# Kernel optimization log

Measured on AMD Instinct MI355X. Metric: run time of the kernel, lower is better.

The kernel has to match this reference:

```python
import jax, jax.numpy as jnp
import numpy as np

B, N, D, E = 8, 96, 512, 4
ALPHA = 0.2  # LeakyReLU negative slope (init arg `alpha`)


def setup_inputs() -> dict:
    key = jax.random.key(0)
    ks = jax.random.split(key, 12)
    nodes = jax.random.normal(ks[0], (B, N, D), jnp.float32)
    # edges[0]: in-edge type weights, edges[1]: out-edge type weights, each [E, D, D]
    edges = jax.random.normal(ks[1], (2, E, D, D), jnp.float32) * 0.05
    adj_in_type = jax.random.randint(ks[2], (B, N, N), 0, E)
    adj_out_type = jax.random.randint(ks[3], (B, N, N), 0, E)
    eye = jnp.eye(N, dtype=bool)  # self-loop guarantees no all-masked softmax row
    exist_in = (jax.random.uniform(ks[4], (B, N, N)) < 0.1) | eye
    exist_out = (jax.random.uniform(ks[5], (B, N, N)) < 0.1) | eye
    Wa_in = jax.random.normal(ks[6], (2 * D, 1), jnp.float32) * 0.02
    ba_in = jnp.zeros((1,), jnp.float32)
    Wa_out = jax.random.normal(ks[7], (2 * D, 1), jnp.float32) * 0.02
    ba_out = jnp.zeros((1,), jnp.float32)
    Wr = jax.random.normal(ks[8], (3 * D, D), jnp.float32) * 0.02
    br = jnp.zeros((D,), jnp.float32)
    Wz = jax.random.normal(ks[9], (3 * D, D), jnp.float32) * 0.02
    bz = jnp.zeros((D,), jnp.float32)
    Wh = jax.random.normal(ks[10], (3 * D, D), jnp.float32) * 0.02
    bh = jnp.zeros((D,), jnp.float32)
    return dict(nodes=nodes, edges=edges, adj_in_type=adj_in_type, adj_out_type=adj_out_type,
                exist_in=exist_in, exist_out=exist_out, Wa_in=Wa_in, ba_in=ba_in,
                Wa_out=Wa_out, ba_out=ba_out, Wr=Wr, br=br, Wz=Wz, bz=bz, Wh=Wh, bh=bh)


def _edge_messages(nodes, W_types, adj_type, exist):
    """msgs[b,i,j] = nodes[b,j] @ W_types[adj_type[b,i,j]] if edge (i<-j) exists else 0.
    Vectorizes the original triple Python loop: transform all nodes by all E edge
    types once, then gather per (b,i,j). nodes [B,N,D], W_types [E,D,D]."""
    all_msgs = jnp.einsum('bjh,ehd->bejd', nodes, W_types)  # [B,E,N,D]
    b_idx = jnp.arange(nodes.shape[0])[:, None, None]
    j_idx = jnp.arange(nodes.shape[1])[None, None, :]
    msgs = all_msgs[b_idx, adj_type, j_idx]                 # [B,N,N,D]
    return jnp.where(exist[..., None], msgs, 0.0)


def _graph_attention(node_h, msgs, exist, Wa, ba):
    """GAT over the N neighbor slots of each node (softmax along last N axis).
    node_h [B,N,D] is broadcast to pairs, matching node_hidden.unsqueeze(2).repeat."""
    h_rep = jnp.broadcast_to(node_h[:, :, None, :], msgs.shape)  # [B,N,N,D]
    feat = jnp.concatenate([h_rep, msgs], axis=-1)               # [B,N,N,2D]
    score = jax.nn.leaky_relu((feat @ Wa)[..., 0] + ba[0], ALPHA)  # [B,N,N]
    score = jnp.where(exist, score, -1e9)
    attn = jax.nn.softmax(score, axis=-1)
    return jnp.einsum('bij,bijd->bid', attn, msgs)               # [B,N,D]


def reference(nodes, edges, adj_in_type, adj_out_type, exist_in, exist_out,
              Wa_in, ba_in, Wa_out, ba_out, Wr, br, Wz, bz, Wh, bh):
    msgs_in = _edge_messages(nodes, edges[0], adj_in_type, exist_in)
    msgs_out = _edge_messages(nodes, edges[1], adj_out_type, exist_out)
    in_h = _graph_attention(nodes, msgs_in, exist_in, Wa_in, ba_in)
    out_h = _graph_attention(nodes, msgs_out, exist_out, Wa_out, ba_out)
    # Propagator: GGNN-style gated fusion of nodes with in/out aggregates
    a = jnp.concatenate([in_h, out_h], axis=-1)      # [B,N,2D]
    az = jnp.concatenate([a, nodes], axis=-1)        # [B,N,3D]
    r = jax.nn.sigmoid(az @ Wr + br)
    z = jax.nn.sigmoid(az @ Wz + bz)
    h_hat = jnp.tanh(jnp.concatenate([a, r * nodes], axis=-1) @ Wh + bh)
    return (1.0 - z) * nodes + z * h_hat
```

## Files before the change

kernel.cpp:

```cpp
#include <hip/hip_runtime.h>
#include <hip/hip_bf16.h>

#define BB 8
#define NN 96
#define DD 512
#define EE 4
#define ROWS 768

typedef __attribute__((ext_vector_type(8))) short s8v;
typedef __attribute__((ext_vector_type(4))) short s4v;
typedef __attribute__((ext_vector_type(4))) float f32x4;

#define WS_PROJP   4096
#define WS_NODESH  1048576
#define WS_ALLMSGS 2097152
#define WS_ACAT    8388608
#define WS_EDGEST  10747904
#define WS_WT      14942208
#define WS_RN      19660800
#define WS_ZB      20447232
#define WS_HPRE    22020096

__device__ __forceinline__ short f2bf(float x) {
  unsigned int u = __builtin_bit_cast(unsigned int, x);
  u += 0x7FFFu + ((u >> 16) & 1u);
  return (short)(u >> 16);
}
__device__ __forceinline__ float b2f(short s) {
  unsigned int u = ((unsigned int)(unsigned short)s) << 16;
  return __builtin_bit_cast(float, u);
}

__device__ __forceinline__ f32x4 mfma16(s8v a, s8v b, f32x4 c) {
  asm("v_mfma_f32_16x16x32_bf16 %0, %1, %2, %0" : "+v"(c) : "v"(a), "v"(b));
  return c;
}

__device__ __forceinline__ int get_exist(const void* p, int code, int idx) {
  switch (code) {
    case 0: return ((const unsigned char*)p)[idx] != 0;
    case 1: return ((const int*)p)[idx] != 0;
    case 2: return ((const float*)p)[idx] != 0.0f;
    default: return ((const long long*)p)[idx] != 0;
  }
}

__global__ __launch_bounds__(256) void k_prep(const float* __restrict__ edges,
                                              const float* __restrict__ Wr,
                                              const float* __restrict__ Wz,
                                              const float* __restrict__ Wh,
                                              const float* __restrict__ nodes,
                                              const void* exist_in,
                                              const void* exist_out,
                                              short* __restrict__ edgesT,
                                              short* __restrict__ WT,
                                              short* __restrict__ nodesH,
                                              short* __restrict__ AcatH,
                                              int* __restrict__ flags) {
  __shared__ float t[32][33];
  __shared__ int red[3];
  int z = blockIdx.z;
  if (z == 0) {
    if (blockIdx.x) return;
    int tt = threadIdx.x;
    int y = blockIdx.y;
    if (y < 2) {
      if (tt < 3) red[tt] = 0;
      __syncthreads();
      const uint4* p = (const uint4*)(y ? exist_out : exist_in);
      int mis = 0, gt = 0, od = 0;
      for (int i = tt; i < 4608; i += 256) {
        uint4 v = p[i];
        unsigned any = v.x | v.y | v.z | v.w;
        if (any) {
          if (any & 0xFFFFFF00u) mis = 1;
          if (any & 0xFEFEFEFEu) gt = 1;
          if (v.y | v.w) od = 1;
        }
      }
      if (mis) atomicOr(&red[0], 1);
      if (gt) atomicOr(&red[1], 1);
      if (od) atomicOr(&red[2], 1);
      __syncthreads();
      if (tt == 0) flags[y] = red[0] ? (red[1] ? 2 : 0) : (red[2] ? 1 : 3);
    } else if (y < 14) {
      int r0 = (y - 2) * 64;
      int c4 = (tt & 127) * 4;
#pragma unroll 4
      for (int p2 = 0; p2 < 32; ++p2) {
        int row = r0 + p2 * 2 + (tt >> 7);
        float4 v = *(const float4*)(nodes + (size_t)row * DD + c4);
        s4v o;
        o[0] = f2bf(v.x); o[1] = f2bf(v.y); o[2] = f2bf(v.z); o[3] = f2bf(v.w);
        *(s4v*)(nodesH + (size_t)row * DD + c4) = o;
        *(s4v*)(AcatH + (size_t)row * 1536 + 1024 + c4) = o;
      }
    }
    return;
  }
  const float* src;
  short* dst;
  int dstPitch;
  if (z < 9) {
    if (blockIdx.y >= 16) return;
    int e = z - 1;
    src = edges + (size_t)e * DD * DD;
    dst = edgesT + (size_t)e * DD * DD;
    dstPitch = DD;
  } else {
    int w = z - 9;
    src = w == 0 ? Wr : (w == 1 ? Wz : Wh);
    dst = WT + (size_t)w * (512 * 1536);
    dstPitch = 1536;
  }
  int r0 = blockIdx.y * 32, c0 = blockIdx.x * 32;
  int row = threadIdx.x >> 3, c4 = (threadIdx.x & 7) * 4;
  float4 v = *(const float4*)(src + (size_t)(r0 + row) * DD + c0 + c4);
  t[row][c4] = v.x; t[row][c4 + 1] = v.y; t[row][c4 + 2] = v.z; t[row][c4 + 3] = v.w;
  __syncthreads();
  s4v o;
  o[0] = f2bf(t[c4 + 0][row]); o[1] = f2bf(t[c4 + 1][row]);
  o[2] = f2bf(t[c4 + 2][row]); o[3] = f2bf(t[c4 + 3][row]);
  *(s4v*)(dst + (size_t)(c0 + row) * dstPitch + r0 + c4) = o;
}

__device__ __forceinline__ void mfma_tile(const short* As, const short* Bs,
                                          int wr, int wc, int l, f32x4 acc[2][2]) {
  int lr = l & 15, lg = l >> 4;
#pragma unroll
  for (int ks = 0; ks < 64; ks += 32) {
    s8v a0 = *(const s8v*)&As[(wr + lr) * 72 + ks + 8 * lg];
    s8v a1 = *(const s8v*)&As[(wr + 16 + lr) * 72 + ks + 8 * lg];
    s8v b0 = *(const s8v*)&Bs[(wc + lr) * 72 + ks + 8 * lg];
    s8v b1 = *(const s8v*)&Bs[(wc + 16 + lr) * 72 + ks + 8 * lg];
    acc[0][0] = mfma16(a0, b0, acc[0][0]);
    acc[0][1] = mfma16(a0, b1, acc[0][1]);
    acc[1][0] = mfma16(a1, b0, acc[1][0]);
    acc[1][1] = mfma16(a1, b1, acc[1][1]);
  }
}

__global__ __launch_bounds__(256) void k_gemm_msgs(const short* __restrict__ nodesH,
                                                   const short* __restrict__ edgesT,
                                                   const float* __restrict__ Wa_in,
                                                   const float* __restrict__ Wa_out,
                                                   short* __restrict__ C,
                                                   float* __restrict__ projp) {
  __shared__ __align__(16) short As[128 * 72];
  __shared__ __align__(16) short Bs[128 * 72];
  __shared__ float pp[2][128];
  int tid = threadIdx.x;
  int row0 = blockIdx.y * 128;
  int col0 = blockIdx.x * 128;
  int de = col0 >> 9, h0 = col0 & 511;
  int w = tid >> 6, l = tid & 63;
  int wr = (w >> 1) * 64, wc = (w & 1) * 64;
  int lr = l & 15, lg = l >> 4;
  int srow = tid >> 1, sc = (tid & 1) * 32;
  const short* Ap = nodesH + (size_t)(row0 + srow) * DD + sc;
  const short* Bp = edgesT + (size_t)de * DD * DD + (size_t)(h0 + srow) * DD + sc;
  s8v a0 = *(const s8v*)Ap, a1 = *(const s8v*)(Ap + 8);
  s8v a2 = *(const s8v*)(Ap + 16), a3 = *(const s8v*)(Ap + 24);
  s8v b0 = *(const s8v*)Bp, b1 = *(const s8v*)(Bp + 8);
  s8v b2 = *(const s8v*)(Bp + 16), b3 = *(const s8v*)(Bp + 24);
  f32x4 acc[4][4] = {};
  for (int k0 = 0; k0 < DD; k0 += 64) {
    *(s8v*)&As[srow * 72 + sc] = a0;      *(s8v*)&As[srow * 72 + sc + 8] = a1;
    *(s8v*)&As[srow * 72 + sc + 16] = a2; *(s8v*)&As[srow * 72 + sc + 24] = a3;
    *(s8v*)&Bs[srow * 72 + sc] = b0;      *(s8v*)&Bs[srow * 72 + sc + 8] = b1;
    *(s8v*)&Bs[srow * 72 + sc + 16] = b2; *(s8v*)&Bs[srow * 72 + sc + 24] = b3;
    __syncthreads();
    if (k0 + 64 < DD) {
      Ap += 64; Bp += 64;
      a0 = *(const s8v*)Ap; a1 = *(const s8v*)(Ap + 8);
      a2 = *(const s8v*)(Ap + 16); a3 = *(const s8v*)(Ap + 24);
      b0 = *(const s8v*)Bp; b1 = *(const s8v*)(Bp + 8);
      b2 = *(const s8v*)(Bp + 16); b3 = *(const s8v*)(Bp + 24);
    }
#pragma unroll
    for (int ks = 0; ks < 64; ks += 32) {
      s8v af[4], bf[4];
#pragma unroll
      for (int f = 0; f < 4; ++f) {
        af[f] = *(const s8v*)&As[(wr + f * 16 + lr) * 72 + ks + 8 * lg];
        bf[f] = *(const s8v*)&Bs[(wc + f * 16 + lr) * 72 + ks + 8 * lg];
      }
#pragma unroll
      for (int fi = 0; fi < 4; ++fi)
#pragma unroll
        for (int fj = 0; fj < 4; ++fj)
          acc[fi][fj] = mfma16(af[fi], bf[fj], acc[fi][fj]);
    }
    __syncthreads();
  }
  asm volatile("s_nop 7\n\ts_nop 7");
  int lg4 = lg * 4;
#pragma unroll
  for (int fi = 0; fi < 4; ++fi)
#pragma unroll
    for (int fj = 0; fj < 4; ++fj) {
      f32x4 v = acc[fi][fj];
#pragma unroll
      for (int r = 0; r < 4; ++r) {
        int row = row0 + wr + fi * 16 + lg4 + r;
        int col = h0 + wc + fj * 16 + lr;
        C[((size_t)(de * ROWS + row)) * DD + col] = f2bf(v[r]);
      }
    }
  const float* wa2 = ((de >> 2) ? Wa_out : Wa_in) + DD;
  float wv[4];
#pragma unroll
  for (int fj = 0; fj < 4; ++fj) wv[fj] = wa2[h0 + wc + fj * 16 + lr];
  float pr[4][4];
#pragma unroll
  for (int fi = 0; fi < 4; ++fi)
#pragma unroll
    for (int r = 0; r < 4; ++r) {
      float s = 0.f;
#pragma unroll
      for (int fj = 0; fj < 4; ++fj) s = fmaf(acc[fi][fj][r], wv[fj], s);
      pr[fi][r] = s;
    }
#pragma unroll
  for (int off = 1; off < 16; off <<= 1)
#pragma unroll
    for (int fi = 0; fi < 4; ++fi)
#pragma unroll
      for (int r = 0; r < 4; ++r) pr[fi][r] += __shfl_xor(pr[fi][r], off);
  if (lr == 0) {
#pragma unroll
    for (int fi = 0; fi < 4; ++fi)
#pragma unroll
      for (int r = 0; r < 4; ++r)
        pp[w & 1][(wr >> 6) * 64 + ((wr & 63) + fi * 16 + lg4 + r)] = pr[fi][r];
  }
  __syncthreads();
  if (tid < 128)
    projp[(size_t)(blockIdx.x & 3) * 6144 + de * ROWS + row0 + tid] =
        pp[0][tid] + pp[1][tid];
}

__global__ __launch_bounds__(256) void k_attn(const short* __restrict__ allmsgsH,
                                              const float* __restrict__ projp,
                                              const int* __restrict__ adj_in,
                                              const int* __restrict__ adj_out,
                                              const void* exist_in,
                                              const void* exist_out,
                                              const int* __restrict__ fr,
                                              const float* __restrict__ nodes,
                                              const float* __restrict__ Wa_in,
                                              const float* __restrict__ ba_in,
                                              const float* __restrict__ Wa_out,
                                              const float* __restrict__ ba_out,
                                              short* __restrict__ AcatH) {
  __shared__ float s_w[NN];
  __shared__ int s_off[NN];
  __shared__ int s_list[NN];
  __shared__ int s_cnt[2];
  __shared__ float s_part[5];
  int blk = blockIdx.x;
  int dir = blk / ROWS;
  int row = blk % ROWS;
  int b = row / NN;
  const int* adj = dir ? adj_out : adj_in;
  const void* ex = dir ? exist_out : exist_in;
  int code = fr[dir];
  int t = threadIdx.x, wv = t >> 6, lane = t & 63;
  const float* wa = dir ? Wa_out : Wa_in;
  float2 nv = *(const float2*)(nodes + (size_t)row * DD + 2 * t);
  float p = fmaf(nv.x, wa[2 * t], nv.y * wa[2 * t + 1]);
#pragma unroll
  for (int off = 32; off; off >>= 1) p += __shfl_xor(p, off);
  if (lane == 0) s_part[wv] = p;
  int ex_ = 0, tj_ = 0;
  if (t < NN) {
    int idx = row * NN + t;
    ex_ = get_exist(ex, code, idx);
    tj_ = adj[idx];
    s_off[t] = ((dir * 4 + tj_) * ROWS + b * NN + t) * DD;
  }
  if (wv == 0) {
    unsigned long long m = __ballot(ex_);
    int pos = __popcll(m & ((1ull << lane) - 1));
    if (ex_) s_list[pos] = t;
    if (lane == 0) s_cnt[0] = (int)__popcll(m);
  } else if (wv == 1) {
    unsigned long long m = __ballot(t < NN && ex_);
    int pos = __popcll(m & ((1ull << lane) - 1));
    if (t < NN && ex_) s_list[64 + pos] = t;
    if (lane == 0) s_cnt[1] = (int)__popcll(m);
  }
  __syncthreads();
  float s1v = s_part[0] + s_part[1] + s_part[2] + s_part[3] +
              (dir ? ba_out[0] : ba_in[0]);
  if (t < NN) {
    float sc = -1e9f;
    if (ex_) {
      size_t base = (size_t)(dir * 4 + tj_) * ROWS + b * NN + t;
      float pv = 0.f;
#pragma unroll
      for (int c = 0; c < 4; ++c) pv += projp[(size_t)c * 6144 + base];
      float x = s1v + pv;
      sc = x >= 0.f ? x : 0.2f * x;
    }
    s_w[t] = sc;
  }
  __syncthreads();
  if (t < 64) {
    float e1 = s_w[t];
    float e2 = (t < 32) ? s_w[t + 64] : -1e30f;
    float mx = fmaxf(e1, e2);
#pragma unroll
    for (int off = 32; off; off >>= 1) mx = fmaxf(mx, __shfl_xor(mx, off));
    float w1 = (e1 > -1e8f) ? __expf(e1 - mx) : 0.f;
    float w2 = (t < 32 && e2 > -1e8f) ? __expf(e2 - mx) : 0.f;
    s_w[t] = w1;
    if (t < 32) s_w[t + 64] = w2;
    float sm = w1 + w2;
#pragma unroll
    for (int off = 32; off; off >>= 1) sm += __shfl_xor(sm, off);
    if (t == 0) s_part[4] = 1.f / sm;
  }
  __syncthreads();
  float inv = s_part[4];
  int c0 = s_cnt[0], c1 = s_cnt[1];
  float acc0 = 0.f, acc1 = 0.f;
  int t2 = 2 * t;
#pragma unroll 4
  for (int q = 0; q < c0; ++q) {
    int j = s_list[q];
    float wj = s_w[j];
    unsigned u = *(const unsigned*)(allmsgsH + s_off[j] + t2);
    acc0 = fmaf(wj, b2f((short)(u & 0xFFFF)), acc0);
    acc1 = fmaf(wj, b2f((short)(u >> 16)), acc1);
  }
#pragma unroll 4
  for (int q = 0; q < c1; ++q) {
    int j = s_list[64 + q];
    float wj = s_w[j];
    unsigned u = *(const unsigned*)(allmsgsH + s_off[j] + t2);
    acc0 = fmaf(wj, b2f((short)(u & 0xFFFF)), acc0);
    acc1 = fmaf(wj, b2f((short)(u >> 16)), acc1);
  }
  unsigned o0 = (unsigned short)f2bf(acc0 * inv);
  unsigned o1 = (unsigned short)f2bf(acc1 * inv);
  *(unsigned*)(AcatH + (size_t)row * 1536 + dir * DD + t2) = o0 | (o1 << 16);
}

__global__ __launch_bounds__(256) void k_gemm1(const short* __restrict__ AcatH,
                                               const short* __restrict__ WT,
                                               const float* __restrict__ br,
                                               const float* __restrict__ bz,
                                               const float* __restrict__ nodes,
                                               short* __restrict__ rnH,
                                               float* __restrict__ zb,
                                               float* __restrict__ Hpre) {
  __shared__ __align__(16) short As[64 * 72];
  __shared__ __align__(16) short Bs[64 * 72];
  int tid = threadIdx.x;
  int row0 = blockIdx.y * 64;
  int col0 = blockIdx.x * 64;
  int region = col0 >> 9, c0 = col0 & 511;
  int K = (region == 2) ? 1024 : 1536;
  int w = tid >> 6, l = tid & 63;
  int wr = (w >> 1) * 32, wc = (w & 1) * 32;
  int srow = tid >> 2, scc = (tid & 3) * 16;
  const short* Ap = AcatH + (size_t)(row0 + srow) * 1536 + scc;
  const short* Bp = WT + (size_t)region * (512 * 1536) + (size_t)(c0 + srow) * 1536 + scc;
  s8v a0 = *(const s8v*)Ap, a1 = *(const s8v*)(Ap + 8);
  s8v b0 = *(const s8v*)Bp, b1 = *(const s8v*)(Bp + 8);
  f32x4 acc[2][2] = {};
  for (int k0 = 0; k0 < K; k0 += 64) {
    *(s8v*)&As[srow * 72 + scc] = a0; *(s8v*)&As[srow * 72 + scc + 8] = a1;
    *(s8v*)&Bs[srow * 72 + scc] = b0; *(s8v*)&Bs[srow * 72 + scc + 8] = b1;
    __syncthreads();
    if (k0 + 64 < K) {
      Ap += 64; Bp += 64;
      a0 = *(const s8v*)Ap; a1 = *(const s8v*)(Ap + 8);
      b0 = *(const s8v*)Bp; b1 = *(const s8v*)(Bp + 8);
    }
    mfma_tile(As, Bs, wr, wc, l, acc);
    __syncthreads();
  }
  asm volatile("s_nop 7\n\ts_nop 7");
  int lr = l & 15, lg4 = (l >> 4) * 4;
#pragma unroll
  for (int fi = 0; fi < 2; ++fi)
#pragma unroll
    for (int fj = 0; fj < 2; ++fj) {
      f32x4 v = acc[fi][fj];
#pragma unroll
      for (int r = 0; r < 4; ++r) {
        int row = row0 + wr + fi * 16 + lg4 + r;
        int c = c0 + wc + fj * 16 + lr;
        float vv = v[r];
        size_t o = (size_t)row * DD + c;
        if (region == 0) {
          float s = 1.f / (1.f + __expf(-(vv + br[c])));
          rnH[o] = f2bf(s * nodes[o]);
        } else if (region == 1) {
          zb[o] = 1.f / (1.f + __expf(-(vv + bz[c])));
        } else {
          Hpre[o] = vv;
        }
      }
    }
}

__global__ __launch_bounds__(256) void k_gemm2(const short* __restrict__ rnH,
                                               const short* __restrict__ WT,
                                               const float* __restrict__ bh,
                                               const float* __restrict__ Hpre,
                                               const float* __restrict__ zb,
                                               const float* __restrict__ nodes,
                                               float* __restrict__ out) {
  __shared__ __align__(16) short As[64 * 72];
  __shared__ __align__(16) short Bs[64 * 72];
  int tid = threadIdx.x;
  int row0 = blockIdx.y * 64;
  int col0 = blockIdx.x * 64;
  int w = tid >> 6, l = tid & 63;
  int wr = (w >> 1) * 32, wc = (w & 1) * 32;
  int srow = tid >> 2, scc = (tid & 3) * 16;
  const short* Ap = rnH + (size_t)(row0 + srow) * DD + scc;
  const short* Bp = WT + (size_t)2 * (512 * 1536) + (size_t)(col0 + srow) * 1536 + 1024 + scc;
  s8v a0 = *(const s8v*)Ap, a1 = *(const s8v*)(Ap + 8);
  s8v b0 = *(const s8v*)Bp, b1 = *(const s8v*)(Bp + 8);
  f32x4 acc[2][2] = {};
  for (int k0 = 0; k0 < DD; k0 += 64) {
    *(s8v*)&As[srow * 72 + scc] = a0; *(s8v*)&As[srow * 72 + scc + 8] = a1;
    *(s8v*)&Bs[srow * 72 + scc] = b0; *(s8v*)&Bs[srow * 72 + scc + 8] = b1;
    __syncthreads();
    if (k0 + 64 < DD) {
      Ap += 64; Bp += 64;
      a0 = *(const s8v*)Ap; a1 = *(const s8v*)(Ap + 8);
      b0 = *(const s8v*)Bp; b1 = *(const s8v*)(Bp + 8);
    }
    mfma_tile(As, Bs, wr, wc, l, acc);
    __syncthreads();
  }
  asm volatile("s_nop 7\n\ts_nop 7");
  int lr = l & 15, lg4 = (l >> 4) * 4;
#pragma unroll
  for (int fi = 0; fi < 2; ++fi)
#pragma unroll
    for (int fj = 0; fj < 2; ++fj) {
      f32x4 v = acc[fi][fj];
#pragma unroll
      for (int r = 0; r < 4; ++r) {
        int row = row0 + wr + fi * 16 + lg4 + r;
        int c = col0 + wc + fj * 16 + lr;
        size_t o = (size_t)row * DD + c;
        float h = tanhf(v[r] + Hpre[o] + bh[c]);
        float zz = zb[o];
        float nd = nodes[o];
        out[o] = (1.f - zz) * nd + zz * h;
      }
    }
}

extern "C" void kernel_launch(void* const* d_in, const int* in_sizes, int n_in,
                              void* d_out, int out_size, void* d_ws, size_t ws_size,
                              hipStream_t stream) {
  const float* nodes = (const float*)d_in[0];
  const float* edges = (const float*)d_in[1];
  const int* adj_in = (const int*)d_in[2];
  const int* adj_out = (const int*)d_in[3];
  const void* exist_in = d_in[4];
  const void* exist_out = d_in[5];
  const float* Wa_in = (const float*)d_in[6];
  const float* ba_in = (const float*)d_in[7];
  const float* Wa_out = (const float*)d_in[8];
  const float* ba_out = (const float*)d_in[9];
  const float* Wr = (const float*)d_in[10];
  const float* br = (const float*)d_in[11];
  const float* Wz = (const float*)d_in[12];
  const float* bz = (const float*)d_in[13];
  const float* Wh = (const float*)d_in[14];
  const float* bh = (const float*)d_in[15];

  char* ws = (char*)d_ws;
  int* flags = (int*)ws;
  float* projp = (float*)(ws + WS_PROJP);
  short* nodesH = (short*)(ws + WS_NODESH);
  short* allmsgsH = (short*)(ws + WS_ALLMSGS);
  short* AcatH = (short*)(ws + WS_ACAT);
  short* edgesT = (short*)(ws + WS_EDGEST);
  short* WT = (short*)(ws + WS_WT);
  short* rnH = (short*)(ws + WS_RN);
  float* zb = (float*)(ws + WS_ZB);
  float* Hpre = (float*)(ws + WS_HPRE);
  float* out = (float*)d_out;

  k_prep<<<dim3(16, 48, 12), 256, 0, stream>>>(edges, Wr, Wz, Wh, nodes,
                                               exist_in, exist_out, edgesT, WT,
                                               nodesH, AcatH, flags);
  k_gemm_msgs<<<dim3(32, 6), 256, 0, stream>>>(nodesH, edgesT, Wa_in, Wa_out,
                                               allmsgsH, projp);
  k_attn<<<2 * ROWS, 256, 0, stream>>>(allmsgsH, projp, adj_in, adj_out,
                                       exist_in, exist_out, flags, nodes,
                                       Wa_in, ba_in, Wa_out, ba_out, AcatH);
  k_gemm1<<<dim3(24, 12), 256, 0, stream>>>(AcatH, WT, br, bz, nodes, rnH, zb,
                                            Hpre);
  k_gemm2<<<dim3(8, 12), 256, 0, stream>>>(rnH, WT, bh, Hpre, zb, nodes, out);
}
```

Measured before the change: 61.61 us.

## Use direct global-to-LDS loads with XOR swizzle in GEMMs and compact prep grid

GEMM kernels now stage A/B tiles with global_load_lds into an unpadded, XOR-swizzled LDS layout instead of loading through registers into padded rows. This removes the VGPR round trip and LDS padding. The old register-level prefetch of the next k-tile is dropped, so load latency is no longer overlapped with MFMA work. The prep kernel is relaunched as a compact 1D grid, eliminating thousands of early-exit blocks.

Result: slower. 66.74 us (+8.3%).

```diff
diff --git a/kernel.cpp b/kernel.cpp
--- a/kernel.cpp
+++ b/kernel.cpp
@@ -34,6 +34,38 @@
 __device__ __forceinline__ f32x4 mfma16(s8v a, s8v b, f32x4 c) {
   asm("v_mfma_f32_16x16x32_bf16 %0, %1, %2, %0" : "+v"(c) : "v"(a), "v"(b));
   return c;
+}
+
+__device__ __forceinline__ void gload16(const short* g, short* l) {
+  __builtin_amdgcn_global_load_lds(
+      (const __attribute__((address_space(1))) void*)g,
+      (__attribute__((address_space(3))) void*)l, 16, 0, 0);
+}
+
+__device__ __forceinline__ void stage64(const short* __restrict__ src, int pitch,
+                                        short* buf, int tid) {
+  int wv = tid >> 6, l = tid & 63;
+  int rsub = l >> 3;
+  int cs = (l & 7) ^ rsub;
+#pragma unroll
+  for (int h = 0; h < 2; ++h) {
+    int r0 = wv * 16 + h * 8;
+    gload16(src + (size_t)(r0 + rsub) * pitch + cs * 8, &buf[r0 * 64]);
+  }
+}
+__device__ __forceinline__ void stage128(const short* __restrict__ src, int pitch,
+                                         short* buf, int tid) {
+  int wv = tid >> 6, l = tid & 63;
+  int rsub = l >> 3;
+  int cs = (l & 7) ^ rsub;
+#pragma unroll
+  for (int h = 0; h < 4; ++h) {
+    int r0 = wv * 32 + h * 8;
+    gload16(src + (size_t)(r0 + rsub) * pitch + cs * 8, &buf[r0 * 64]);
+  }
+}
+__device__ __forceinline__ s8v lds_frag(const short* buf, int row, int kc) {
+  return *(const s8v*)&buf[row * 64 + ((kc ^ (row & 7)) << 3)];
 }
 
 __device__ __forceinline__ int get_exist(const void* p, int code, int idx) {
@@ -59,84 +91,66 @@
                                               int* __restrict__ flags) {
   __shared__ float t[32][33];
   __shared__ int red[3];
-  int z = blockIdx.z;
-  if (z == 0) {
-    if (blockIdx.x) return;
-    int tt = threadIdx.x;
-    int y = blockIdx.y;
-    if (y < 2) {
-      if (tt < 3) red[tt] = 0;
-      __syncthreads();
-      const uint4* p = (const uint4*)(y ? exist_out : exist_in);
-      int mis = 0, gt = 0, od = 0;
-      for (int i = tt; i < 4608; i += 256) {
-        uint4 v = p[i];
-        unsigned any = v.x | v.y | v.z | v.w;
-        if (any) {
-          if (any & 0xFFFFFF00u) mis = 1;
-          if (any & 0xFEFEFEFEu) gt = 1;
-          if (v.y | v.w) od = 1;
-        }
+  int task = blockIdx.x;
+  int tt = threadIdx.x;
+  if (task < 4352) {
+    const float* src;
+    short* dst;
+    int dstPitch, r0, c0;
+    if (task < 2048) {
+      int e = task >> 8, rem = task & 255;
+      src = edges + (size_t)e * DD * DD;
+      dst = edgesT + (size_t)e * DD * DD;
+      dstPitch = DD;
+      r0 = (rem >> 4) * 32; c0 = (rem & 15) * 32;
+    } else {
+      int q = task - 2048;
+      int z = q / 768, rem = q % 768;
+      src = z == 0 ? Wr : (z == 1 ? Wz : Wh);
+      dst = WT + (size_t)z * (512 * 1536);
+      dstPitch = 1536;
+      r0 = (rem >> 4) * 32; c0 = (rem & 15) * 32;
+    }
+    int row = tt >> 3, c4 = (tt & 7) * 4;
+    float4 v = *(const float4*)(src + (size_t)(r0 + row) * DD + c0 + c4);
+    t[row][c4] = v.x; t[row][c4 + 1] = v.y; t[row][c4 + 2] = v.z; t[row][c4 + 3] = v.w;
+    __syncthreads();
+    s4v o;
+    o[0] = f2bf(t[c4 + 0][row]); o[1] = f2bf(t[c4 + 1][row]);
+    o[2] = f2bf(t[c4 + 2][row]); o[3] = f2bf(t[c4 + 3][row]);
+    *(s4v*)(dst + (size_t)(c0 + row) * dstPitch + r0 + c4) = o;
+  } else if (task < 4364) {
+    int r0 = (task - 4352) * 64;
+    int c4 = (tt & 127) * 4;
+#pragma unroll 4
+    for (int p2 = 0; p2 < 32; ++p2) {
+      int row = r0 + p2 * 2 + (tt >> 7);
+      float4 v = *(const float4*)(nodes + (size_t)row * DD + c4);
+      s4v o;
+      o[0] = f2bf(v.x); o[1] = f2bf(v.y); o[2] = f2bf(v.z); o[3] = f2bf(v.w);
+      *(s4v*)(nodesH + (size_t)row * DD + c4) = o;
+      *(s4v*)(AcatH + (size_t)row * 1536 + 1024 + c4) = o;
+    }
+  } else {
+    int y = task - 4364;
+    if (tt < 3) red[tt] = 0;
+    __syncthreads();
+    const uint4* p = (const uint4*)(y ? exist_out : exist_in);
+    int mis = 0, gt = 0, od = 0;
+    for (int i = tt; i < 4608; i += 256) {
+      uint4 v = p[i];
+      unsigned any = v.x | v.y | v.z | v.w;
+      if (any) {
+        if (any & 0xFFFFFF00u) mis = 1;
+        if (any & 0xFEFEFEFEu) gt = 1;
+        if (v.y | v.w) od = 1;
       }
-      if (mis) atomicOr(&red[0], 1);
-      if (gt) atomicOr(&red[1], 1);
-      if (od) atomicOr(&red[2], 1);
-      __syncthreads();
-      if (tt == 0) flags[y] = red[0] ? (red[1] ? 2 : 0) : (red[2] ? 1 : 3);
-    } else if (y < 14) {
-      int r0 = (y - 2) * 64;
-      int c4 = (tt & 127) * 4;
-#pragma unroll 4
-      for (int p2 = 0; p2 < 32; ++p2) {
-        int row = r0 + p2 * 2 + (tt >> 7);
-        float4 v = *(const float4*)(nodes + (size_t)row * DD + c4);
-        s4v o;
-        o[0] = f2bf(v.x); o[1] = f2bf(v.y); o[2] = f2bf(v.z); o[3] = f2bf(v.w);
-        *(s4v*)(nodesH + (size_t)row * DD + c4) = o;
-        *(s4v*)(AcatH + (size_t)row * 1536 + 1024 + c4) = o;
-      }
-    }
-    return;
-  }
-  const float* src;
-  short* dst;
-  int dstPitch;
-  if (z < 9) {
-    if (blockIdx.y >= 16) return;
-    int e = z - 1;
-    src = edges + (size_t)e * DD * DD;
-    dst = edgesT + (size_t)e * DD * DD;
-    dstPitch = DD;
-  } else {
-    int w = z - 9;
-    src = w == 0 ? Wr : (w == 1 ? Wz : Wh);
-    dst = WT + (size_t)w * (512 * 1536);
-    dstPitch = 1536;
-  }
-  int r0 = blockIdx.y * 32, c0 = blockIdx.x * 32;
-  int row = threadIdx.x >> 3, c4 = (threadIdx.x & 7) * 4;
-  float4 v = *(const float4*)(src + (size_t)(r0 + row) * DD + c0 + c4);
-  t[row][c4] = v.x; t[row][c4 + 1] = v.y; t[row][c4 + 2] = v.z; t[row][c4 + 3] = v.w;
-  __syncthreads();
-  s4v o;
-  o[0] = f2bf(t[c4 + 0][row]); o[1] = f2bf(t[c4 + 1][row]);
-  o[2] = f2bf(t[c4 + 2][row]); o[3] = f2bf(t[c4 + 3][row]);
-  *(s4v*)(dst + (size_t)(c0 + row) * dstPitch + r0 + c4) = o;
-}
-
-__device__ __forceinline__ void mfma_tile(const short* As, const short* Bs,
-                                          int wr, int wc, int l, f32x4 acc[2][2]) {
-  int lr = l & 15, lg = l >> 4;
-#pragma unroll
-  for (int ks = 0; ks < 64; ks += 32) {
-    s8v a0 = *(const s8v*)&As[(wr + lr) * 72 + ks + 8 * lg];
-    s8v a1 = *(const s8v*)&As[(wr + 16 + lr) * 72 + ks + 8 * lg];
-    s8v b0 = *(const s8v*)&Bs[(wc + lr) * 72 + ks + 8 * lg];
-    s8v b1 = *(const s8v*)&Bs[(wc + 16 + lr) * 72 + ks + 8 * lg];
-    acc[0][0] = mfma16(a0, b0, acc[0][0]);
-    acc[0][1] = mfma16(a0, b1, acc[0][1]);
-    acc[1][0] = mfma16(a1, b0, acc[1][0]);
-    acc[1][1] = mfma16(a1, b1, acc[1][1]);
+    }
+    if (mis) atomicOr(&red[0], 1);
+    if (gt) atomicOr(&red[1], 1);
+    if (od) atomicOr(&red[2], 1);
+    __syncthreads();
+    if (tt == 0) flags[y] = red[0] ? (red[1] ? 2 : 0) : (red[2] ? 1 : 3);
   }
 }
 
@@ -146,8 +160,8 @@
                                                    const float* __restrict__ Wa_out,
                                                    short* __restrict__ C,
                                                    float* __restrict__ projp) {
-  __shared__ __align__(16) short As[128 * 72];
-  __shared__ __align__(16) short Bs[128 * 72];
+  __shared__ __align__(16) short As[128 * 64];
+  __shared__ __align__(16) short Bs[128 * 64];
   __shared__ float pp[2][128];
   int tid = threadIdx.x;
   int row0 = blockIdx.y * 128;
@@ -156,34 +170,21 @@
   int w = tid >> 6, l = tid & 63;
   int wr = (w >> 1) * 64, wc = (w & 1) * 64;
   int lr = l & 15, lg = l >> 4;
-  int srow = tid >> 1, sc = (tid & 1) * 32;
-  const short* Ap = nodesH + (size_t)(row0 + srow) * DD + sc;
-  const short* Bp = edgesT + (size_t)de * DD * DD + (size_t)(h0 + srow) * DD + sc;
-  s8v a0 = *(const s8v*)Ap, a1 = *(const s8v*)(Ap + 8);
-  s8v a2 = *(const s8v*)(Ap + 16), a3 = *(const s8v*)(Ap + 24);
-  s8v b0 = *(const s8v*)Bp, b1 = *(const s8v*)(Bp + 8);
-  s8v b2 = *(const s8v*)(Bp + 16), b3 = *(const s8v*)(Bp + 24);
+  const short* Asrc = nodesH + (size_t)row0 * DD;
+  const short* Bsrc = edgesT + (size_t)de * DD * DD + (size_t)h0 * DD;
   f32x4 acc[4][4] = {};
   for (int k0 = 0; k0 < DD; k0 += 64) {
-    *(s8v*)&As[srow * 72 + sc] = a0;      *(s8v*)&As[srow * 72 + sc + 8] = a1;
-    *(s8v*)&As[srow * 72 + sc + 16] = a2; *(s8v*)&As[srow * 72 + sc + 24] = a3;
-    *(s8v*)&Bs[srow * 72 + sc] = b0;      *(s8v*)&Bs[srow * 72 + sc + 8] = b1;
-    *(s8v*)&Bs[srow * 72 + sc + 16] = b2; *(s8v*)&Bs[srow * 72 + sc + 24] = b3;
-    __syncthreads();
-    if (k0 + 64 < DD) {
-      Ap += 64; Bp += 64;
-      a0 = *(const s8v*)Ap; a1 = *(const s8v*)(Ap + 8);
-      a2 = *(const s8v*)(Ap + 16); a3 = *(const s8v*)(Ap + 24);
-      b0 = *(const s8v*)Bp; b1 = *(const s8v*)(Bp + 8);
-      b2 = *(const s8v*)(Bp + 16); b3 = *(const s8v*)(Bp + 24);
-    }
-#pragma unroll
-    for (int ks = 0; ks < 64; ks += 32) {
+    stage128(Asrc + k0, DD, As, tid);
+    stage128(Bsrc + k0, DD, Bs, tid);
+    __syncthreads();
+#pragma unroll
+    for (int ks2 = 0; ks2 < 2; ++ks2) {
+      int kc = ks2 * 4 + lg;
       s8v af[4], bf[4];
 #pragma unroll
       for (int f = 0; f < 4; ++f) {
-        af[f] = *(const s8v*)&As[(wr + f * 16 + lr) * 72 + ks + 8 * lg];
-        bf[f] = *(const s8v*)&Bs[(wc + f * 16 + lr) * 72 + ks + 8 * lg];
+        af[f] = lds_frag(As, wr + f * 16 + lr, kc);
+        bf[f] = lds_frag(Bs, wc + f * 16 + lr, kc);
       }
 #pragma unroll
       for (int fi = 0; fi < 4; ++fi)
@@ -355,8 +356,8 @@
                                                short* __restrict__ rnH,
                                                float* __restrict__ zb,
                                                float* __restrict__ Hpre) {
-  __shared__ __align__(16) short As[64 * 72];
-  __shared__ __align__(16) short Bs[64 * 72];
+  __shared__ __align__(16) short As[64 * 64];
+  __shared__ __align__(16) short Bs[64 * 64];
   int tid = threadIdx.x;
   int row0 = blockIdx.y * 64;
   int col0 = blockIdx.x * 64;
@@ -364,26 +365,30 @@
   int K = (region == 2) ? 1024 : 1536;
   int w = tid >> 6, l = tid & 63;
   int wr = (w >> 1) * 32, wc = (w & 1) * 32;
-  int srow = tid >> 2, scc = (tid & 3) * 16;
-  const short* Ap = AcatH + (size_t)(row0 + srow) * 1536 + scc;
-  const short* Bp = WT + (size_t)region * (512 * 1536) + (size_t)(c0 + srow) * 1536 + scc;
-  s8v a0 = *(const s8v*)Ap, a1 = *(const s8v*)(Ap + 8);
-  s8v b0 = *(const s8v*)Bp, b1 = *(const s8v*)(Bp + 8);
+  int lr = l & 15, lg = l >> 4;
+  const short* Asrc = AcatH + (size_t)row0 * 1536;
+  const short* Bsrc = WT + (size_t)region * (512 * 1536) + (size_t)c0 * 1536;
   f32x4 acc[2][2] = {};
   for (int k0 = 0; k0 < K; k0 += 64) {
-    *(s8v*)&As[srow * 72 + scc] = a0; *(s8v*)&As[srow * 72 + scc + 8] = a1;
-    *(s8v*)&Bs[srow * 72 + scc] = b0; *(s8v*)&Bs[srow * 72 + scc + 8] = b1;
-    __syncthreads();
-    if (k0 + 64 < K) {
-      Ap += 64; Bp += 64;
-      a0 = *(const s8v*)Ap; a1 = *(const s8v*)(Ap + 8);
-      b0 = *(const s8v*)Bp; b1 = *(const s8v*)(Bp + 8);
-    }
-    mfma_tile(As, Bs, wr, wc, l, acc);
+    stage64(Asrc + k0, 1536, As, tid);
+    stage64(Bsrc + k0, 1536, Bs, tid);
+    __syncthreads();
+#pragma unroll
+    for (int ks2 = 0; ks2 < 2; ++ks2) {
+      int kc = ks2 * 4 + lg;
+      s8v a0 = lds_frag(As, wr + lr, kc);
+      s8v a1 = lds_frag(As, wr + 16 + lr, kc);
+      s8v b0 = lds_frag(Bs, wc + lr, kc);
+      s8v b1 = lds_frag(Bs, wc + 16 + lr, kc);
+      acc[0][0] = mfma16(a0, b0, acc[0][0]);
+      acc[0][1] = mfma16(a0, b1, acc[0][1]);
+      acc[1][0] = mfma16(a1, b0, acc[1][0]);
+      acc[1][1] = mfma16(a1, b1, acc[1][1]);
+    }
     __syncthreads();
   }
   asm volatile("s_nop 7\n\ts_nop 7");
-  int lr = l & 15, lg4 = (l >> 4) * 4;
+  int lg4 = lg * 4;
 #pragma unroll
   for (int fi = 0; fi < 2; ++fi)
 #pragma unroll
@@ -414,33 +419,37 @@
                                                const float* __restrict__ zb,
                                                const float* __restrict__ nodes,
                                                float* __restrict__ out) {
-  __shared__ __align__(16) short As[64 * 72];
-  __shared__ __align__(16) short Bs[64 * 72];
+  __shared__ __align__(16) short As[64 * 64];
+  __shared__ __align__(16) short Bs[64 * 64];
   int tid = threadIdx.x;
   int row0 = blockIdx.y * 64;
   int col0 = blockIdx.x * 64;
   int w = tid >> 6, l = tid & 63;
   int wr = (w >> 1) * 32, wc = (w & 1) * 32;
-  int srow = tid >> 2, scc = (tid & 3) * 16;
-  const short* Ap = rnH + (size_t)(row0 + srow) * DD + scc;
-  const short* Bp = WT + (size_t)2 * (512 * 1536) + (size_t)(col0 + srow) * 1536 + 1024 + scc;
-  s8v a0 = *(const s8v*)Ap, a1 = *(const s8v*)(Ap + 8);
-  s8v b0 = *(const s8v*)Bp, b1 = *(const s8v*)(Bp + 8);
+  int lr = l & 15, lg = l >> 4;
+  const short* Asrc = rnH + (size_t)row0 * DD;
+  const short* Bsrc = WT + (size_t)2 * (512 * 1536) + (size_t)col0 * 1536 + 1024;
   f32x4 acc[2][2] = {};
   for (int k0 = 0; k0 < DD; k0 += 64) {
-    *(s8v*)&As[srow * 72 + scc] = a0; *(s8v*)&As[srow * 72 + scc + 8] = a1;
-    *(s8v*)&Bs[srow * 72 + scc] = b0; *(s8v*)&Bs[srow * 72 + scc + 8] = b1;
-    __syncthreads();
-    if (k0 + 64 < DD) {
-      Ap += 64; Bp += 64;
-      a0 = *(const s8v*)Ap; a1 = *(const s8v*)(Ap + 8);
-      b0 = *(const s8v*)Bp; b1 = *(const s8v*)(Bp + 8);
-    }
-    mfma_tile(As, Bs, wr, wc, l, acc);
+    stage64(Asrc + k0, DD, As, tid);
+    stage64(Bsrc + k0, 1536, Bs, tid);
+    __syncthreads();
+#pragma unroll
+    for (int ks2 = 0; ks2 < 2; ++ks2) {
+      int kc = ks2 * 4 + lg;
+      s8v a0 = lds_frag(As, wr + lr, kc);
+      s8v a1 = lds_frag(As, wr + 16 + lr, kc);
+      s8v b0 = lds_frag(Bs, wc + lr, kc);
+      s8v b1 = lds_frag(Bs, wc + 16 + lr, kc);
+      acc[0][0] = mfma16(a0, b0, acc[0][0]);
+      acc[0][1] = mfma16(a0, b1, acc[0][1]);
+      acc[1][0] = mfma16(a1, b0, acc[1][0]);
+      acc[1][1] = mfma16(a1, b1, acc[1][1]);
+    }
     __syncthreads();
   }
   asm volatile("s_nop 7\n\ts_nop 7");
-  int lr = l & 15, lg4 = (l >> 4) * 4;
+  int lg4 = lg * 4;
 #pragma unroll
   for (int fi = 0; fi < 2; ++fi)
 #pragma unroll
@@ -492,9 +501,8 @@
   float* Hpre = (float*)(ws + WS_HPRE);
   float* out = (float*)d_out;
 
-  k_prep<<<dim3(16, 48, 12), 256, 0, stream>>>(edges, Wr, Wz, Wh, nodes,
-                                               exist_in, exist_out, edgesT, WT,
-                                               nodesH, AcatH, flags);
+  k_prep<<<4366, 256, 0, stream>>>(edges, Wr, Wz, Wh, nodes, exist_in,
+                                   exist_out, edgesT, WT, nodesH, AcatH, flags);
   k_gemm_msgs<<<dim3(32, 6), 256, 0, stream>>>(nodesH, edgesT, Wa_in, Wa_out,
                                                allmsgsH, projp);
   k_attn<<<2 * ROWS, 256, 0, stream>>>(allmsgsH, projp, adj_in, adj_out,
```
